# Performance work log

Measured on AMD Instinct MI355X. Metric: run time of the kernel, lower is better.

Reference implementation:

```python
import jax, jax.numpy as jnp
import numpy as np

N_HEADS = 16
PROJ_DIM = 64  # per-head dim
DIM = N_HEADS * PROJ_DIM  # 1024


def setup_inputs() -> dict:
    key = jax.random.key(0)
    k1, k2, k3, k4, k5 = jax.random.split(key, 5)
    N, L = 2, 2048
    scale = 1.0 / np.sqrt(DIM)
    return {
        "query": jax.random.normal(k1, (N, L, DIM), dtype=jnp.float32),
        "key": jax.random.normal(k2, (N, L, DIM), dtype=jnp.float32),
        "Wq": jax.random.normal(k3, (DIM, DIM), dtype=jnp.float32) * scale,
        "Wk": jax.random.normal(k4, (DIM, DIM), dtype=jnp.float32) * scale,
        "Wv": jax.random.normal(k5, (DIM, DIM), dtype=jnp.float32) * scale,
    }


def reference(query, key, Wq, Wk, Wv):
    # Causal linear-complexity attention (mask=True branch, left_first=False).
    N, Lq, _ = query.shape
    Lk = key.shape[1]
    H, Dh = N_HEADS, PROJ_DIM
    # torch Linear: x @ W.T ; reshape to (N, H, L, Dh)
    q = (query @ Wq.T).reshape(N, Lq, H, Dh).transpose(0, 2, 1, 3)
    k = (key @ Wk.T).reshape(N, Lk, H, Dh).transpose(0, 2, 1, 3)
    v = (key @ Wv.T).reshape(N, Lk, H, Dh).transpose(0, 2, 1, 3)
    q = jax.nn.softmax(q, axis=-1)
    k = jax.nn.softmax(k, axis=-1)
    # right[t] = sum_{s<=t} k_s^T v_s  : (N,H,Lk,Dh,Dh) cumulative outer products
    S = jnp.cumsum(jnp.einsum('nhti,nhtj->nhtij', k, v), axis=2)
    out = jnp.einsum('nhti,nhtij->nhtj', q, S)  # (N,H,Lq,Dh)
    return out.transpose(0, 2, 1, 3).reshape(N, Lq, H * Dh)
```

## Files before the change

kernel.cpp:

```cpp
#include <hip/hip_runtime.h>


constexpr int DIM  = 1024;
constexpr int H    = 16;
constexpr int DH   = 64;
constexpr int LSEQ = 2048;
constexpr int NB   = 2;
constexpr int MTOK = NB * LSEQ;
constexpr int CS   = 64;
constexpr int NC   = LSEQ / CS;

typedef __bf16 bf16x8 __attribute__((ext_vector_type(8)));
typedef float floatx4 __attribute__((ext_vector_type(4)));
typedef unsigned short ushort_t;

__device__ __forceinline__ ushort_t f2bf(float f) {
  unsigned int u = __float_as_uint(f);
  u += 0x7FFFu + ((u >> 16) & 1u);
  return (ushort_t)(u >> 16);
}

__device__ __forceinline__ void async16(void* lds, const void* g) {
  __builtin_amdgcn_global_load_lds(
      (const __attribute__((address_space(1))) unsigned int*)g,
      (__attribute__((address_space(3))) unsigned int*)lds, 16, 0, 0);
}

__device__ __forceinline__ bf16x8 tfrag(const unsigned int* T, int row, int uoff) {
  union { bf16x8 v; unsigned int u[4]; } r;
  const unsigned int* p = T + row * 33 + uoff;
  r.u[0] = p[0]; r.u[1] = p[1]; r.u[2] = p[2]; r.u[3] = p[3];
  return r.v;
}

__device__ __forceinline__ void transpose_tile(const ushort_t* g, unsigned int* TT, int tid) {
  const int ic = tid & 7, tp = tid >> 3;
  const ushort_t* r0 = g + (size_t)(2 * tp) * DIM + ic * 8;
  union { uint4 q; ushort_t u[8]; } a0, a1;
  a0.q = *(const uint4*)r0;
  a1.q = *(const uint4*)(r0 + DIM);
#pragma unroll
  for (int j = 0; j < 8; j++)
    TT[(8 * ic + j) * 33 + tp] = (unsigned int)a0.u[j] | ((unsigned int)a1.u[j] << 16);
}

__global__ __launch_bounds__(256) void cast_all(const float* __restrict__ q,
                                                const float* __restrict__ k,
                                                const float* __restrict__ wq,
                                                const float* __restrict__ wk,
                                                const float* __restrict__ wv,
                                                ushort_t* __restrict__ xbf,
                                                ushort_t* __restrict__ wbf) {
  const int seg = blockIdx.y;
  const float* src;
  ushort_t* dst;
  int n4;
  if (seg == 0)      { src = q;  dst = xbf;                  n4 = (4 << 20) / 4; }
  else if (seg == 1) { src = k;  dst = xbf + (4 << 20);      n4 = (4 << 20) / 4; }
  else if (seg == 2) { src = wq; dst = wbf;                  n4 = (1 << 20) / 4; }
  else if (seg == 3) { src = wk; dst = wbf + (1 << 20);      n4 = (1 << 20) / 4; }
  else               { src = wv; dst = wbf + (2 << 20);      n4 = (1 << 20) / 4; }
  for (int i = blockIdx.x * 256 + threadIdx.x; i < n4; i += gridDim.x * 256) {
    const float4 f = ((const float4*)src)[i];
    ((ushort4*)dst)[i] = make_ushort4(f2bf(f.x), f2bf(f.y), f2bf(f.z), f2bf(f.w));
  }
}

__global__ __launch_bounds__(512, 2) void gemm_fused(const ushort_t* __restrict__ xbf,
                                                     const ushort_t* __restrict__ wbf,
                                                     ushort_t* __restrict__ qp,
                                                     ushort_t* __restrict__ kp,
                                                     ushort_t* __restrict__ vp) {
  __shared__ __align__(16) ushort_t sh[65536];
  const int tid = threadIdx.x;

  const int xcd   = blockIdx.x & 7;
  const int local = blockIdx.x >> 3;
  const int T     = xcd * 24 + local;
  const int z     = T >> 6;
  const int rem   = T & 63;
  const int bm    = (rem >> 2) * 256;
  const int bn    = (rem & 3) * 256;

  const ushort_t* A = xbf + (z ? (size_t)(4 << 20) : 0);
  const ushort_t* W = wbf + (size_t)z * (1 << 20);
  ushort_t* C = (z == 0) ? qp : ((z == 1) ? kp : vp);

  const int lane  = tid & 63;
  const int wid   = tid >> 6;
  const int wr    = wid >> 2, wc = wid & 3;
  const int row16 = lane & 15, quad = lane >> 4;

  floatx4 acc[8][4] = {};

  const int srow = tid >> 3;
  const int lc   = (tid & 7) ^ (srow & 7);
  const ushort_t* pA[2][2];
  const ushort_t* pB[2][2];
#pragma unroll
  for (int h = 0; h < 2; h++)
#pragma unroll
    for (int rnd = 0; rnd < 2; rnd++) {
      pA[h][rnd] = A + (size_t)(bm + h * 128 + rnd * 64 + srow) * DIM + lc * 8;
      pB[h][rnd] = W + (size_t)(bn + h * 128 + rnd * 64 + srow) * DIM + lc * 8;
    }
  char* shW = (char*)sh;

#define STG(b, ism, h, kt)                                          \
  {                                                                 \
    char* d_ = shW + (b) * 65536 + (ism) * 32768 + (h) * 16384 + tid * 16; \
    async16(d_,        ((ism) ? pB : pA)[h][0] + (size_t)(kt) * 64);       \
    async16(d_ + 8192, ((ism) ? pB : pA)[h][1] + (size_t)(kt) * 64);       \
  }

  const int key = row16 & 7;
  const int xc0 = (quad ^ key) * 16;
  const int xc1 = ((4 + quad) ^ key) * 16;
  const int aOff = wr * 16384 + row16 * 128;
  const int bOff = 32768 + (wc >> 1) * 16384 + (wc & 1) * 8192 + row16 * 128;
  const char* shR = (const char*)sh;

  bf16x8 aF[4][2], bF[4][2];

#define RD_A4(p, base)                                                        \
  {                                                                           \
    _Pragma("unroll")                                                         \
    for (int mt = 0; mt < 4; mt++) {                                          \
      aF[mt][0] = *(const bf16x8*)(shR + (p) * 65536 + aOff + ((base) + mt) * 2048 + xc0); \
      aF[mt][1] = *(const bf16x8*)(shR + (p) * 65536 + aOff + ((base) + mt) * 2048 + xc1); \
    }                                                                         \
  }
#define RD_B2(p, base)                                                        \
  {                                                                           \
    _Pragma("unroll")                                                         \
    for (int j = 0; j < 2; j++) {                                             \
      bF[(base) + j][0] = *(const bf16x8*)(shR + (p) * 65536 + bOff + ((base) + j) * 2048 + xc0); \
      bF[(base) + j][1] = *(const bf16x8*)(shR + (p) * 65536 + bOff + ((base) + j) * 2048 + xc1); \
    }                                                                         \
  }
#define MFMA8(mb, nb)                                                         \
  {                                                                           \
    _Pragma("unroll")                                                         \
    for (int mt = 0; mt < 4; mt++)                                            \
      _Pragma("unroll")                                                       \
      for (int nt = 0; nt < 2; nt++) {                                        \
        acc[(mb) + mt][(nb) + nt] = __builtin_amdgcn_mfma_f32_16x16x32_bf16(  \
            aF[mt][0], bF[(nb) + nt][0], acc[(mb) + mt][(nb) + nt], 0, 0, 0); \
        acc[(mb) + mt][(nb) + nt] = __builtin_amdgcn_mfma_f32_16x16x32_bf16(  \
            aF[mt][1], bF[(nb) + nt][1], acc[(mb) + mt][(nb) + nt], 0, 0, 0); \
      }                                                                       \
  }
#define BARD()  asm volatile("s_barrier" ::: "memory")
#define LGKM0() asm volatile("s_waitcnt lgkmcnt(0)" ::: "memory")

  STG(0, 0, 0, 0); STG(0, 1, 0, 0);
  STG(0, 1, 1, 0); STG(0, 0, 1, 0);
  STG(1, 0, 0, 1); STG(1, 1, 0, 1);
  asm volatile("s_waitcnt vmcnt(4)" ::: "memory");
  BARD();

  for (int u = 0; u < 16; ++u) {
    const int p  = u & 1;
    const int qb = p ^ 1;
    RD_A4(p, 0); RD_B2(p, 0);
    if (u + 1 < 16) { STG(qb, 1, 1, u + 1); STG(qb, 0, 1, u + 1); }
    BARD(); LGKM0();
    __builtin_amdgcn_s_setprio(1); MFMA8(0, 0); __builtin_amdgcn_s_setprio(0);
    BARD();
    RD_B2(p, 2);
    BARD(); LGKM0();
    __builtin_amdgcn_s_setprio(1); MFMA8(0, 2); __builtin_amdgcn_s_setprio(0);
    BARD();
    RD_A4(p, 4);
    BARD(); LGKM0();
    __builtin_amdgcn_s_setprio(1); MFMA8(4, 0); __builtin_amdgcn_s_setprio(0);
    BARD();
    if (u + 2 < 16) {
      STG(p, 0, 0, u + 2); STG(p, 1, 0, u + 2);
      asm volatile("s_waitcnt vmcnt(4)" ::: "memory");
    } else {
      asm volatile("s_waitcnt vmcnt(0)" ::: "memory");
    }
    BARD();
    __builtin_amdgcn_s_setprio(1); MFMA8(4, 2); __builtin_amdgcn_s_setprio(0);
    BARD();
  }
#undef STG
#undef RD_A4
#undef RD_B2
#undef MFMA8
#undef BARD
#undef LGKM0
  __syncthreads();

  if (z < 2) {
#pragma unroll
    for (int mt = 0; mt < 8; mt++)
#pragma unroll
      for (int r = 0; r < 4; r++) {
        float m = fmaxf(fmaxf(acc[mt][0][r], acc[mt][1][r]),
                        fmaxf(acc[mt][2][r], acc[mt][3][r]));
#pragma unroll
        for (int o = 1; o < 16; o <<= 1) m = fmaxf(m, __shfl_xor(m, o, 64));
        float e[4], s = 0.f;
#pragma unroll
        for (int nt = 0; nt < 4; nt++) { e[nt] = __expf(acc[mt][nt][r] - m); s += e[nt]; }
#pragma unroll
        for (int o = 1; o < 16; o <<= 1) s += __shfl_xor(s, o, 64);
        const float inv = 1.f / s;
#pragma unroll
        for (int nt = 0; nt < 4; nt++) acc[mt][nt][r] = e[nt] * inv;
      }
  }

  ushort_t* CsB = sh;
#pragma unroll
  for (int p4 = 0; p4 < 4; ++p4) {
    __syncthreads();
    if (wr == (p4 >> 1)) {
      const int mh = (p4 & 1) * 4;
#pragma unroll
      for (int m4 = 0; m4 < 4; m4++)
#pragma unroll
        for (int nt = 0; nt < 4; nt++)
#pragma unroll
          for (int r = 0; r < 4; r++)
            CsB[(m4 * 16 + quad * 4 + r) * 264 + wc * 64 + nt * 16 + row16] =
                f2bf(acc[mh + m4][nt][r]);
    }
    __syncthreads();
#pragma unroll
    for (int it = 0; it < 4; it++) {
      const int ch = tid + it * 512;
      const int row = ch >> 5, ic = ch & 31;
      *(uint4*)&C[(size_t)(bm + p4 * 64 + row) * DIM + bn + ic * 8] =
          *(const uint4*)&CsB[row * 264 + ic * 8];
    }
  }
}

__global__ __launch_bounds__(256) void chunk_T(const ushort_t* __restrict__ kp,
                                               const ushort_t* __restrict__ vp,
                                               float* __restrict__ cs) {
  __shared__ unsigned int KT[64 * 33];
  __shared__ unsigned int VT[64 * 33];
  const int c = blockIdx.x, h = blockIdx.y, n = blockIdx.z;
  const int tid = threadIdx.x;
  const size_t gbase = ((size_t)(n * LSEQ + c * CS)) * DIM + h * DH;

  transpose_tile(kp + gbase, KT, tid);
  transpose_tile(vp + gbase, VT, tid);
  __syncthreads();

  const int lane = tid & 63, wid = tid >> 6;
  const int row16 = lane & 15, quad = lane >> 4;

  floatx4 acc[4] = {};
#pragma unroll
  for (int ks = 0; ks < 2; ks++) {
    const bf16x8 a = tfrag(VT, wid * 16 + row16, ks * 16 + quad * 4);
#pragma unroll
    for (int nt = 0; nt < 4; nt++) {
      const bf16x8 b = tfrag(KT, nt * 16 + row16, ks * 16 + quad * 4);
      acc[nt] = __builtin_amdgcn_mfma_f32_16x16x32_bf16(a, b, acc[nt], 0, 0, 0);
    }
  }
  float* outp = cs + ((size_t)((n * H + h) * NC + c)) * (DH * DH);
#pragma unroll
  for (int nt = 0; nt < 4; nt++)
#pragma unroll
    for (int r = 0; r < 4; r++)
      outp[(wid * 16 + quad * 4 + r) * DH + nt * 16 + row16] = acc[nt][r];
}

__global__ __launch_bounds__(256) void prefix_chunks(const float* __restrict__ cs,
                                                     ushort_t* __restrict__ csb) {
  const int nh = blockIdx.x >> 4;
  const int e  = (blockIdx.x & 15) * 256 + threadIdx.x;
  const float* bf_ = cs + (size_t)nh * NC * (DH * DH) + e;
  ushort_t* bb = csb + (size_t)nh * NC * (DH * DH) + e;
  float run = 0.f;
#pragma unroll
  for (int c = 0; c < NC; c++) {
    const float cur = bf_[(size_t)c * (DH * DH)];
    bb[(size_t)c * (DH * DH)] = f2bf(run);
    run += cur;
  }
}

__global__ __launch_bounds__(256) void attn_mfma(const ushort_t* __restrict__ qp,
                                                 const ushort_t* __restrict__ kp,
                                                 const ushort_t* __restrict__ vp,
                                                 const ushort_t* __restrict__ csb,
                                                 float* __restrict__ out) {
  __shared__ ushort_t Qs[64 * 72];
  __shared__ ushort_t Ks[64 * 72];
  __shared__ ushort_t Ts[64 * 72];
  __shared__ unsigned int VT[64 * 33];
  __shared__ ushort_t Pb[64 * 72];
  const int c = blockIdx.x, h = blockIdx.y, n = blockIdx.z;
  const int tid = threadIdx.x;
  const size_t gbase = ((size_t)(n * LSEQ + c * CS)) * DIM + h * DH;
  const size_t cbase = ((size_t)((n * H + h) * NC + c)) * (DH * DH);

#pragma unroll
  for (int it = 0; it < 2; it++) {
    const int ch = tid + it * 256;
    const int row = ch >> 3, ic = ch & 7;
    *(uint4*)&Qs[row * 72 + ic * 8] = *(const uint4*)&qp[gbase + (size_t)row * DIM + ic * 8];
    *(uint4*)&Ks[row * 72 + ic * 8] = *(const uint4*)&kp[gbase + (size_t)row * DIM + ic * 8];
    *(uint4*)&Ts[row * 72 + ic * 8] = *(const uint4*)&csb[cbase + (size_t)row * DH + ic * 8];
  }
  transpose_tile(vp + gbase, VT, tid);
  __syncthreads();

  const int lane = tid & 63, wid = tid >> 6;
  const int row16 = lane & 15, quad = lane >> 4;
  const int t0 = wid * 16;

  floatx4 acc[4] = {};
  floatx4 pacc[4] = {};

#pragma unroll
  for (int ks = 0; ks < 2; ks++) {
    const bf16x8 aq = *(const bf16x8*)&Qs[(t0 + row16) * 72 + ks * 32 + quad * 8];
#pragma unroll
    for (int nt = 0; nt < 4; nt++) {
      const bf16x8 bt = *(const bf16x8*)&Ts[(nt * 16 + row16) * 72 + ks * 32 + quad * 8];
      acc[nt] = __builtin_amdgcn_mfma_f32_16x16x32_bf16(aq, bt, acc[nt], 0, 0, 0);
      const bf16x8 bk = *(const bf16x8*)&Ks[(nt * 16 + row16) * 72 + ks * 32 + quad * 8];
      pacc[nt] = __builtin_amdgcn_mfma_f32_16x16x32_bf16(aq, bk, pacc[nt], 0, 0, 0);
    }
  }
#pragma unroll
  for (int nt = 0; nt < 4; nt++)
#pragma unroll
    for (int r = 0; r < 4; r++) {
      const int t = t0 + quad * 4 + r, s = nt * 16 + row16;
      Pb[t * 72 + s] = f2bf((s <= t) ? pacc[nt][r] : 0.f);
    }
  __syncthreads();

#pragma unroll
  for (int ks = 0; ks < 2; ks++) {
    const bf16x8 ap = *(const bf16x8*)&Pb[(t0 + row16) * 72 + ks * 32 + quad * 8];
#pragma unroll
    for (int nt = 0; nt < 4; nt++) {
      const bf16x8 bv = tfrag(VT, nt * 16 + row16, ks * 16 + quad * 4);
      acc[nt] = __builtin_amdgcn_mfma_f32_16x16x32_bf16(ap, bv, acc[nt], 0, 0, 0);
    }
  }

#pragma unroll
  for (int nt = 0; nt < 4; nt++)
#pragma unroll
    for (int r = 0; r < 4; r++)
      out[gbase + (size_t)(t0 + quad * 4 + r) * DIM + nt * 16 + row16] = acc[nt][r];
}

extern "C" void kernel_launch(void* const* d_in, const int* in_sizes, int n_in,
                              void* d_out, int out_size, void* d_ws, size_t ws_size,
                              hipStream_t stream) {
  const float* query = (const float*)d_in[0];
  const float* key   = (const float*)d_in[1];
  const float* Wq    = (const float*)d_in[2];
  const float* Wk    = (const float*)d_in[3];
  const float* Wv    = (const float*)d_in[4];
  float* out = (float*)d_out;

  const size_t PM = (size_t)4 << 20;
  ushort_t* qp = (ushort_t*)d_ws;
  ushort_t* kp = qp + PM;
  ushort_t* vp = kp + PM;
  float*    cs = (float*)(vp + PM);
  ushort_t* csb = (ushort_t*)(cs + PM);
  ushort_t* xbf = (ushort_t*)cs;
  ushort_t* wbf = (ushort_t*)out;

  cast_all<<<dim3(512, 5), 256, 0, stream>>>(query, key, Wq, Wk, Wv, xbf, wbf);

  gemm_fused<<<dim3(192), 512, 0, stream>>>(xbf, wbf, qp, kp, vp);

  chunk_T<<<dim3(NC, H, NB), 256, 0, stream>>>(kp, vp, cs);
  prefix_chunks<<<dim3(NB * H * 16), 256, 0, stream>>>(cs, csb);
  attn_mfma<<<dim3(NC, H, NB), 256, 0, stream>>>(qp, kp, vp, csb, out);
}
```

Baseline: 158.5 us.

## Simplify GEMM main loop to per-stage double buffering and batch prefix loads

```diff
diff --git a/kernel.cpp b/kernel.cpp
--- a/kernel.cpp
+++ b/kernel.cpp
@@ -106,12 +106,14 @@
     }
   char* shW = (char*)sh;
 
-#define STG(b, ism, h, kt)                                          \
+#define STG1(b, ism, h, kt)                                         \
   {                                                                 \
     char* d_ = shW + (b) * 65536 + (ism) * 32768 + (h) * 16384 + tid * 16; \
     async16(d_,        ((ism) ? pB : pA)[h][0] + (size_t)(kt) * 64);       \
     async16(d_ + 8192, ((ism) ? pB : pA)[h][1] + (size_t)(kt) * 64);       \
   }
+#define STG4(b, kt)                                                 \
+  { STG1(b, 0, 0, kt); STG1(b, 1, 0, kt); STG1(b, 0, 1, kt); STG1(b, 1, 1, kt); }
 
   const int key = row16 & 7;
   const int xc0 = (quad ^ key) * 16;
@@ -122,75 +124,66 @@
 
   bf16x8 aF[4][2], bF[4][2];
 
-#define RD_A4(p, base)                                                        \
+#define RD_A4(bp, base)                                                       \
   {                                                                           \
     _Pragma("unroll")                                                         \
     for (int mt = 0; mt < 4; mt++) {                                          \
-      aF[mt][0] = *(const bf16x8*)(shR + (p) * 65536 + aOff + ((base) + mt) * 2048 + xc0); \
-      aF[mt][1] = *(const bf16x8*)(shR + (p) * 65536 + aOff + ((base) + mt) * 2048 + xc1); \
+      aF[mt][0] = *(const bf16x8*)((bp) + aOff + ((base) + mt) * 2048 + xc0); \
+      aF[mt][1] = *(const bf16x8*)((bp) + aOff + ((base) + mt) * 2048 + xc1); \
     }                                                                         \
   }
-#define RD_B2(p, base)                                                        \
+#define RD_B4(bp)                                                             \
   {                                                                           \
     _Pragma("unroll")                                                         \
-    for (int j = 0; j < 2; j++) {                                             \
-      bF[(base) + j][0] = *(const bf16x8*)(shR + (p) * 65536 + bOff + ((base) + j) * 2048 + xc0); \
-      bF[(base) + j][1] = *(const bf16x8*)(shR + (p) * 65536 + bOff + ((base) + j) * 2048 + xc1); \
+    for (int j = 0; j < 4; j++) {                                             \
+      bF[j][0] = *(const bf16x8*)((bp) + bOff + j * 2048 + xc0);              \
+      bF[j][1] = *(const bf16x8*)((bp) + bOff + j * 2048 + xc1);              \
     }                                                                         \
   }
-#define MFMA8(mb, nb)                                                         \
+#define MFMA32(mb)                                                            \
   {                                                                           \
     _Pragma("unroll")                                                         \
     for (int mt = 0; mt < 4; mt++)                                            \
       _Pragma("unroll")                                                       \
-      for (int nt = 0; nt < 2; nt++) {                                        \
-        acc[(mb) + mt][(nb) + nt] = __builtin_amdgcn_mfma_f32_16x16x32_bf16(  \
-            aF[mt][0], bF[(nb) + nt][0], acc[(mb) + mt][(nb) + nt], 0, 0, 0); \
-        acc[(mb) + mt][(nb) + nt] = __builtin_amdgcn_mfma_f32_16x16x32_bf16(  \
-            aF[mt][1], bF[(nb) + nt][1], acc[(mb) + mt][(nb) + nt], 0, 0, 0); \
+      for (int nt = 0; nt < 4; nt++) {                                        \
+        acc[(mb) + mt][nt] = __builtin_amdgcn_mfma_f32_16x16x32_bf16(         \
+            aF[mt][0], bF[nt][0], acc[(mb) + mt][nt], 0, 0, 0);               \
+        acc[(mb) + mt][nt] = __builtin_amdgcn_mfma_f32_16x16x32_bf16(         \
+            aF[mt][1], bF[nt][1], acc[(mb) + mt][nt], 0, 0, 0);               \
       }                                                                       \
   }
-#define BARD()  asm volatile("s_barrier" ::: "memory")
-#define LGKM0() asm volatile("s_waitcnt lgkmcnt(0)" ::: "memory")
-
-  STG(0, 0, 0, 0); STG(0, 1, 0, 0);
-  STG(0, 1, 1, 0); STG(0, 0, 1, 0);
-  STG(1, 0, 0, 1); STG(1, 1, 0, 1);
-  asm volatile("s_waitcnt vmcnt(4)" ::: "memory");
-  BARD();
+
+  STG4(0, 0);
 
   for (int u = 0; u < 16; ++u) {
-    const int p  = u & 1;
-    const int qb = p ^ 1;
-    RD_A4(p, 0); RD_B2(p, 0);
-    if (u + 1 < 16) { STG(qb, 1, 1, u + 1); STG(qb, 0, 1, u + 1); }
-    BARD(); LGKM0();
-    __builtin_amdgcn_s_setprio(1); MFMA8(0, 0); __builtin_amdgcn_s_setprio(0);
-    BARD();
-    RD_B2(p, 2);
-    BARD(); LGKM0();
-    __builtin_amdgcn_s_setprio(1); MFMA8(0, 2); __builtin_amdgcn_s_setprio(0);
-    BARD();
-    RD_A4(p, 4);
-    BARD(); LGKM0();
-    __builtin_amdgcn_s_setprio(1); MFMA8(4, 0); __builtin_amdgcn_s_setprio(0);
-    BARD();
-    if (u + 2 < 16) {
-      STG(p, 0, 0, u + 2); STG(p, 1, 0, u + 2);
-      asm volatile("s_waitcnt vmcnt(4)" ::: "memory");
+    const int p = u & 1;
+    __builtin_amdgcn_sched_barrier(0);
+    asm volatile("s_waitcnt lgkmcnt(0)" ::: "memory");
+    __builtin_amdgcn_sched_barrier(0);
+    asm volatile("s_barrier" ::: "memory");
+    if (u + 1 < 16) {
+      STG4(p ^ 1, u + 1);
+      asm volatile("s_waitcnt vmcnt(8)" ::: "memory");
     } else {
       asm volatile("s_waitcnt vmcnt(0)" ::: "memory");
     }
-    BARD();
-    __builtin_amdgcn_s_setprio(1); MFMA8(4, 2); __builtin_amdgcn_s_setprio(0);
-    BARD();
-  }
-#undef STG
+    asm volatile("s_barrier" ::: "memory");
+    const char* bp = shR + p * 65536;
+    RD_A4(bp, 0);
+    RD_B4(bp);
+    __builtin_amdgcn_s_setprio(1);
+    MFMA32(0);
+    __builtin_amdgcn_s_setprio(0);
+    RD_A4(bp, 4);
+    __builtin_amdgcn_s_setprio(1);
+    MFMA32(4);
+    __builtin_amdgcn_s_setprio(0);
+  }
+#undef STG1
+#undef STG4
 #undef RD_A4
-#undef RD_B2
-#undef MFMA8
-#undef BARD
-#undef LGKM0
+#undef RD_B4
+#undef MFMA32
   __syncthreads();
 
   if (z < 2) {
@@ -279,12 +272,14 @@
   const int e  = (blockIdx.x & 15) * 256 + threadIdx.x;
   const float* bf_ = cs + (size_t)nh * NC * (DH * DH) + e;
   ushort_t* bb = csb + (size_t)nh * NC * (DH * DH) + e;
+  float v[NC];
+#pragma unroll
+  for (int c = 0; c < NC; c++) v[c] = bf_[(size_t)c * (DH * DH)];
   float run = 0.f;
 #pragma unroll
   for (int c = 0; c < NC; c++) {
-    const float cur = bf_[(size_t)c * (DH * DH)];
     bb[(size_t)c * (DH * DH)] = f2bf(run);
-    run += cur;
+    run += v[c];
   }
 }
 
```

New measurement: 159.0 us. No clear change (+0.3%).

## Replace chunk-prefix pass with two-level segmented scan fused into attention

Applied to the files above, without the earlier changes.

```diff
diff --git a/kernel.cpp b/kernel.cpp
--- a/kernel.cpp
+++ b/kernel.cpp
@@ -9,6 +9,8 @@
 constexpr int MTOK = NB * LSEQ;
 constexpr int CS   = 64;
 constexpr int NC   = LSEQ / CS;
+constexpr int SEG  = 8;
+constexpr int CPS  = NC / SEG;
 
 typedef __bf16 bf16x8 __attribute__((ext_vector_type(8)));
 typedef float floatx4 __attribute__((ext_vector_type(4)));
@@ -239,123 +241,159 @@
   }
 }
 
-__global__ __launch_bounds__(256) void chunk_T(const ushort_t* __restrict__ kp,
-                                               const ushort_t* __restrict__ vp,
-                                               float* __restrict__ cs) {
+__global__ __launch_bounds__(256) void seg_T(const ushort_t* __restrict__ kp,
+                                             const ushort_t* __restrict__ vp,
+                                             float* __restrict__ cs,
+                                             float* __restrict__ segtot) {
   __shared__ unsigned int KT[64 * 33];
   __shared__ unsigned int VT[64 * 33];
-  const int c = blockIdx.x, h = blockIdx.y, n = blockIdx.z;
+  const int s = blockIdx.x, h = blockIdx.y, n = blockIdx.z;
   const int tid = threadIdx.x;
-  const size_t gbase = ((size_t)(n * LSEQ + c * CS)) * DIM + h * DH;
-
-  transpose_tile(kp + gbase, KT, tid);
-  transpose_tile(vp + gbase, VT, tid);
-  __syncthreads();
-
   const int lane = tid & 63, wid = tid >> 6;
   const int row16 = lane & 15, quad = lane >> 4;
-
-  floatx4 acc[4] = {};
-#pragma unroll
-  for (int ks = 0; ks < 2; ks++) {
-    const bf16x8 a = tfrag(VT, wid * 16 + row16, ks * 16 + quad * 4);
-#pragma unroll
-    for (int nt = 0; nt < 4; nt++) {
-      const bf16x8 b = tfrag(KT, nt * 16 + row16, ks * 16 + quad * 4);
-      acc[nt] = __builtin_amdgcn_mfma_f32_16x16x32_bf16(a, b, acc[nt], 0, 0, 0);
-    }
-  }
-  float* outp = cs + ((size_t)((n * H + h) * NC + c)) * (DH * DH);
+  const int nh = n * H + h;
+
+  floatx4 run[4] = {};
+  for (int j = 0; j < CPS; j++) {
+    const int c = s * CPS + j;
+    const size_t gbase = ((size_t)(n * LSEQ + c * CS)) * DIM + h * DH;
+    if (j) __syncthreads();
+    transpose_tile(kp + gbase, KT, tid);
+    transpose_tile(vp + gbase, VT, tid);
+    __syncthreads();
+
+    floatx4 tacc[4] = {};
+#pragma unroll
+    for (int ks = 0; ks < 2; ks++) {
+      const bf16x8 a = tfrag(VT, wid * 16 + row16, ks * 16 + quad * 4);
+#pragma unroll
+      for (int nt = 0; nt < 4; nt++) {
+        const bf16x8 b = tfrag(KT, nt * 16 + row16, ks * 16 + quad * 4);
+        tacc[nt] = __builtin_amdgcn_mfma_f32_16x16x32_bf16(a, b, tacc[nt], 0, 0, 0);
+      }
+    }
+    float* outp = cs + ((size_t)(nh * NC + c)) * (DH * DH);
+#pragma unroll
+    for (int nt = 0; nt < 4; nt++)
+#pragma unroll
+      for (int r = 0; r < 4; r++)
+        outp[(wid * 16 + quad * 4 + r) * DH + nt * 16 + row16] = run[nt][r];
+#pragma unroll
+    for (int nt = 0; nt < 4; nt++) run[nt] += tacc[nt];
+  }
+  float* st = segtot + ((size_t)(nh * SEG + s)) * (DH * DH);
 #pragma unroll
   for (int nt = 0; nt < 4; nt++)
 #pragma unroll
     for (int r = 0; r < 4; r++)
-      outp[(wid * 16 + quad * 4 + r) * DH + nt * 16 + row16] = acc[nt][r];
-}
-
-__global__ __launch_bounds__(256) void prefix_chunks(const float* __restrict__ cs,
-                                                     ushort_t* __restrict__ csb) {
-  const int nh = blockIdx.x >> 4;
-  const int e  = (blockIdx.x & 15) * 256 + threadIdx.x;
-  const float* bf_ = cs + (size_t)nh * NC * (DH * DH) + e;
-  ushort_t* bb = csb + (size_t)nh * NC * (DH * DH) + e;
-  float run = 0.f;
-#pragma unroll
-  for (int c = 0; c < NC; c++) {
-    const float cur = bf_[(size_t)c * (DH * DH)];
-    bb[(size_t)c * (DH * DH)] = f2bf(run);
-    run += cur;
-  }
-}
-
-__global__ __launch_bounds__(256) void attn_mfma(const ushort_t* __restrict__ qp,
-                                                 const ushort_t* __restrict__ kp,
-                                                 const ushort_t* __restrict__ vp,
-                                                 const ushort_t* __restrict__ csb,
-                                                 float* __restrict__ out) {
-  __shared__ ushort_t Qs[64 * 72];
-  __shared__ ushort_t Ks[64 * 72];
-  __shared__ ushort_t Ts[64 * 72];
-  __shared__ unsigned int VT[64 * 33];
-  __shared__ ushort_t Pb[64 * 72];
-  const int c = blockIdx.x, h = blockIdx.y, n = blockIdx.z;
+      st[(wid * 16 + quad * 4 + r) * DH + nt * 16 + row16] = run[nt][r];
+}
+
+__global__ __launch_bounds__(512) void attn2(const ushort_t* __restrict__ qp,
+                                             const ushort_t* __restrict__ kp,
+                                             const ushort_t* __restrict__ vp,
+                                             const float* __restrict__ cs,
+                                             const float* __restrict__ segtot,
+                                             float* __restrict__ out) {
+  __shared__ float Sb[DH * DH];
+  __shared__ ushort_t Qs[2][64 * 72];
+  __shared__ ushort_t Ks[2][64 * 72];
+  __shared__ ushort_t Ts[2][64 * 72];
+  __shared__ ushort_t Pb[2][64 * 72];
+  __shared__ unsigned int VT2[2][64 * 33];
+  const int s = blockIdx.x, h = blockIdx.y, n = blockIdx.z;
   const int tid = threadIdx.x;
-  const size_t gbase = ((size_t)(n * LSEQ + c * CS)) * DIM + h * DH;
-  const size_t cbase = ((size_t)((n * H + h) * NC + c)) * (DH * DH);
-
-#pragma unroll
-  for (int it = 0; it < 2; it++) {
-    const int ch = tid + it * 256;
-    const int row = ch >> 3, ic = ch & 7;
-    *(uint4*)&Qs[row * 72 + ic * 8] = *(const uint4*)&qp[gbase + (size_t)row * DIM + ic * 8];
-    *(uint4*)&Ks[row * 72 + ic * 8] = *(const uint4*)&kp[gbase + (size_t)row * DIM + ic * 8];
-    *(uint4*)&Ts[row * 72 + ic * 8] = *(const uint4*)&csb[cbase + (size_t)row * DH + ic * 8];
-  }
-  transpose_tile(vp + gbase, VT, tid);
+  const int half = tid >> 8;
+  const int t8   = tid & 255;
+  const int lane = tid & 63;
+  const int wl   = (tid >> 6) & 3;
+  const int row16 = lane & 15, quad = lane >> 4;
+  const int nh = n * H + h;
+
+  {
+    float a8[8] = {0.f, 0.f, 0.f, 0.f, 0.f, 0.f, 0.f, 0.f};
+    const float* base = segtot + (size_t)nh * SEG * (DH * DH) + tid * 8;
+    for (int sp = 0; sp < s; sp++) {
+      const float4 u0 = *(const float4*)(base + (size_t)sp * (DH * DH));
+      const float4 u1 = *(const float4*)(base + (size_t)sp * (DH * DH) + 4);
+      a8[0] += u0.x; a8[1] += u0.y; a8[2] += u0.z; a8[3] += u0.w;
+      a8[4] += u1.x; a8[5] += u1.y; a8[6] += u1.z; a8[7] += u1.w;
+    }
+#pragma unroll
+    for (int i = 0; i < 8; i++) Sb[tid * 8 + i] = a8[i];
+  }
   __syncthreads();
 
-  const int lane = tid & 63, wid = tid >> 6;
-  const int row16 = lane & 15, quad = lane >> 4;
-  const int t0 = wid * 16;
-
-  floatx4 acc[4] = {};
-  floatx4 pacc[4] = {};
-
-#pragma unroll
-  for (int ks = 0; ks < 2; ks++) {
-    const bf16x8 aq = *(const bf16x8*)&Qs[(t0 + row16) * 72 + ks * 32 + quad * 8];
-#pragma unroll
-    for (int nt = 0; nt < 4; nt++) {
-      const bf16x8 bt = *(const bf16x8*)&Ts[(nt * 16 + row16) * 72 + ks * 32 + quad * 8];
-      acc[nt] = __builtin_amdgcn_mfma_f32_16x16x32_bf16(aq, bt, acc[nt], 0, 0, 0);
-      const bf16x8 bk = *(const bf16x8*)&Ks[(nt * 16 + row16) * 72 + ks * 32 + quad * 8];
-      pacc[nt] = __builtin_amdgcn_mfma_f32_16x16x32_bf16(aq, bk, pacc[nt], 0, 0, 0);
-    }
-  }
-#pragma unroll
-  for (int nt = 0; nt < 4; nt++)
-#pragma unroll
-    for (int r = 0; r < 4; r++) {
-      const int t = t0 + quad * 4 + r, s = nt * 16 + row16;
-      Pb[t * 72 + s] = f2bf((s <= t) ? pacc[nt][r] : 0.f);
-    }
-  __syncthreads();
-
-#pragma unroll
-  for (int ks = 0; ks < 2; ks++) {
-    const bf16x8 ap = *(const bf16x8*)&Pb[(t0 + row16) * 72 + ks * 32 + quad * 8];
-#pragma unroll
-    for (int nt = 0; nt < 4; nt++) {
-      const bf16x8 bv = tfrag(VT, nt * 16 + row16, ks * 16 + quad * 4);
-      acc[nt] = __builtin_amdgcn_mfma_f32_16x16x32_bf16(ap, bv, acc[nt], 0, 0, 0);
-    }
-  }
-
-#pragma unroll
-  for (int nt = 0; nt < 4; nt++)
-#pragma unroll
-    for (int r = 0; r < 4; r++)
-      out[gbase + (size_t)(t0 + quad * 4 + r) * DIM + nt * 16 + row16] = acc[nt][r];
+  for (int r2 = 0; r2 < 2; r2++) {
+    const int c = s * CPS + r2 * 2 + half;
+    const size_t gbase = ((size_t)(n * LSEQ + c * CS)) * DIM + h * DH;
+    const float* Pc = cs + ((size_t)(nh * NC + c)) * (DH * DH);
+    if (r2) __syncthreads();
+
+#pragma unroll
+    for (int it = 0; it < 2; it++) {
+      const int ch = t8 + it * 256;
+      const int row = ch >> 3, ic = ch & 7;
+      *(uint4*)&Qs[half][row * 72 + ic * 8] =
+          *(const uint4*)&qp[gbase + (size_t)row * DIM + ic * 8];
+      *(uint4*)&Ks[half][row * 72 + ic * 8] =
+          *(const uint4*)&kp[gbase + (size_t)row * DIM + ic * 8];
+    }
+    transpose_tile(vp + gbase, VT2[half], t8);
+#pragma unroll
+    for (int ii = 0; ii < 2; ii++) {
+      const int e = (t8 + ii * 256) * 8;
+      const int row = e >> 6, col = e & 63;
+      const float4 p0 = *(const float4*)(Pc + e);
+      const float4 p1 = *(const float4*)(Pc + e + 4);
+      ushort_t* d = &Ts[half][row * 72 + col];
+      *(ushort4*)d = make_ushort4(f2bf(p0.x + Sb[e]),     f2bf(p0.y + Sb[e + 1]),
+                                  f2bf(p0.z + Sb[e + 2]), f2bf(p0.w + Sb[e + 3]));
+      *(ushort4*)(d + 4) = make_ushort4(f2bf(p1.x + Sb[e + 4]), f2bf(p1.y + Sb[e + 5]),
+                                        f2bf(p1.z + Sb[e + 6]), f2bf(p1.w + Sb[e + 7]));
+    }
+    __syncthreads();
+
+    const int t0 = wl * 16;
+    floatx4 acc[4] = {};
+    floatx4 pacc[4] = {};
+
+#pragma unroll
+    for (int ks = 0; ks < 2; ks++) {
+      const bf16x8 aq = *(const bf16x8*)&Qs[half][(t0 + row16) * 72 + ks * 32 + quad * 8];
+#pragma unroll
+      for (int nt = 0; nt < 4; nt++) {
+        const bf16x8 bt = *(const bf16x8*)&Ts[half][(nt * 16 + row16) * 72 + ks * 32 + quad * 8];
+        acc[nt] = __builtin_amdgcn_mfma_f32_16x16x32_bf16(aq, bt, acc[nt], 0, 0, 0);
+        const bf16x8 bk = *(const bf16x8*)&Ks[half][(nt * 16 + row16) * 72 + ks * 32 + quad * 8];
+        pacc[nt] = __builtin_amdgcn_mfma_f32_16x16x32_bf16(aq, bk, pacc[nt], 0, 0, 0);
+      }
+    }
+#pragma unroll
+    for (int nt = 0; nt < 4; nt++)
+#pragma unroll
+      for (int r = 0; r < 4; r++) {
+        const int tt = t0 + quad * 4 + r, ss = nt * 16 + row16;
+        Pb[half][tt * 72 + ss] = f2bf((ss <= tt) ? pacc[nt][r] : 0.f);
+      }
+    __syncthreads();
+
+#pragma unroll
+    for (int ks = 0; ks < 2; ks++) {
+      const bf16x8 ap = *(const bf16x8*)&Pb[half][(t0 + row16) * 72 + ks * 32 + quad * 8];
+#pragma unroll
+      for (int nt = 0; nt < 4; nt++) {
+        const bf16x8 bv = tfrag(VT2[half], nt * 16 + row16, ks * 16 + quad * 4);
+        acc[nt] = __builtin_amdgcn_mfma_f32_16x16x32_bf16(ap, bv, acc[nt], 0, 0, 0);
+      }
+    }
+
+#pragma unroll
+    for (int nt = 0; nt < 4; nt++)
+#pragma unroll
+      for (int r = 0; r < 4; r++)
+        out[gbase + (size_t)(t0 + quad * 4 + r) * DIM + nt * 16 + row16] = acc[nt][r];
+  }
 }
 
 extern "C" void kernel_launch(void* const* d_in, const int* in_sizes, int n_in,
@@ -373,7 +411,7 @@
   ushort_t* kp = qp + PM;
   ushort_t* vp = kp + PM;
   float*    cs = (float*)(vp + PM);
-  ushort_t* csb = (ushort_t*)(cs + PM);
+  float*    segtot = cs + PM;
   ushort_t* xbf = (ushort_t*)cs;
   ushort_t* wbf = (ushort_t*)out;
 
@@ -381,7 +419,7 @@
 
   gemm_fused<<<dim3(192), 512, 0, stream>>>(xbf, wbf, qp, kp, vp);
 
-  chunk_T<<<dim3(NC, H, NB), 256, 0, stream>>>(kp, vp, cs);
-  prefix_chunks<<<dim3(NB * H * 16), 256, 0, stream>>>(cs, csb);
-  attn_mfma<<<dim3(NC, H, NB), 256, 0, stream>>>(qp, kp, vp, csb, out);
-}
+  seg_T<<<dim3(SEG, H, NB), 256, 0, stream>>>(kp, vp, cs, segtot);
+
+  attn2<<<dim3(SEG, H, NB), 512, 0, stream>>>(qp, kp, vp, cs, segtot, out);
+}
```

Measured after the change: 156.2 us (median of 2 runs). No clear change (-1.5%).

## Fuse chunk prefix sum into attention kernel by recomputing prior chunk states

Applied to the files above, without the earlier changes.

```diff
diff --git a/kernel.cpp b/kernel.cpp
--- a/kernel.cpp
+++ b/kernel.cpp
@@ -241,7 +241,7 @@
 
 __global__ __launch_bounds__(256) void chunk_T(const ushort_t* __restrict__ kp,
                                                const ushort_t* __restrict__ vp,
-                                               float* __restrict__ cs) {
+                                               float* __restrict__ ct) {
   __shared__ unsigned int KT[64 * 33];
   __shared__ unsigned int VT[64 * 33];
   const int c = blockIdx.x, h = blockIdx.y, n = blockIdx.z;
@@ -265,7 +265,7 @@
       acc[nt] = __builtin_amdgcn_mfma_f32_16x16x32_bf16(a, b, acc[nt], 0, 0, 0);
     }
   }
-  float* outp = cs + ((size_t)((n * H + h) * NC + c)) * (DH * DH);
+  float* outp = ct + ((size_t)((n * H + h) * NC + c)) * (DH * DH);
 #pragma unroll
   for (int nt = 0; nt < 4; nt++)
 #pragma unroll
@@ -273,35 +273,41 @@
       outp[(wid * 16 + quad * 4 + r) * DH + nt * 16 + row16] = acc[nt][r];
 }
 
-__global__ __launch_bounds__(256) void prefix_chunks(const float* __restrict__ cs,
-                                                     ushort_t* __restrict__ csb) {
-  const int nh = blockIdx.x >> 4;
-  const int e  = (blockIdx.x & 15) * 256 + threadIdx.x;
-  const float* bf_ = cs + (size_t)nh * NC * (DH * DH) + e;
-  ushort_t* bb = csb + (size_t)nh * NC * (DH * DH) + e;
-  float run = 0.f;
-#pragma unroll
-  for (int c = 0; c < NC; c++) {
-    const float cur = bf_[(size_t)c * (DH * DH)];
-    bb[(size_t)c * (DH * DH)] = f2bf(run);
-    run += cur;
-  }
-}
-
-__global__ __launch_bounds__(256) void attn_mfma(const ushort_t* __restrict__ qp,
-                                                 const ushort_t* __restrict__ kp,
-                                                 const ushort_t* __restrict__ vp,
-                                                 const ushort_t* __restrict__ csb,
-                                                 float* __restrict__ out) {
+__global__ __launch_bounds__(256) void attn4(const ushort_t* __restrict__ qp,
+                                             const ushort_t* __restrict__ kp,
+                                             const ushort_t* __restrict__ vp,
+                                             const float* __restrict__ ct,
+                                             float* __restrict__ out) {
   __shared__ ushort_t Qs[64 * 72];
   __shared__ ushort_t Ks[64 * 72];
   __shared__ ushort_t Ts[64 * 72];
+  __shared__ ushort_t Pb[64 * 72];
   __shared__ unsigned int VT[64 * 33];
-  __shared__ ushort_t Pb[64 * 72];
   const int c = blockIdx.x, h = blockIdx.y, n = blockIdx.z;
   const int tid = threadIdx.x;
+  const int lane = tid & 63, wid = tid >> 6;
+  const int row16 = lane & 15, quad = lane >> 4;
+  const int nh = n * H + h;
   const size_t gbase = ((size_t)(n * LSEQ + c * CS)) * DIM + h * DH;
-  const size_t cbase = ((size_t)((n * H + h) * NC + c)) * (DH * DH);
+
+  float sb[16] = {0.f, 0.f, 0.f, 0.f, 0.f, 0.f, 0.f, 0.f,
+                  0.f, 0.f, 0.f, 0.f, 0.f, 0.f, 0.f, 0.f};
+  {
+    const float* base = ct + (size_t)nh * NC * (DH * DH);
+    for (int cp = 0; cp < c; cp++) {
+      const float* bsp = base + (size_t)cp * (DH * DH);
+#pragma unroll
+      for (int ii = 0; ii < 2; ii++) {
+        const int e = (tid + ii * 256) * 8;
+        const float4 u0 = *(const float4*)(bsp + e);
+        const float4 u1 = *(const float4*)(bsp + e + 4);
+        sb[ii * 8 + 0] += u0.x; sb[ii * 8 + 1] += u0.y;
+        sb[ii * 8 + 2] += u0.z; sb[ii * 8 + 3] += u0.w;
+        sb[ii * 8 + 4] += u1.x; sb[ii * 8 + 5] += u1.y;
+        sb[ii * 8 + 6] += u1.z; sb[ii * 8 + 7] += u1.w;
+      }
+    }
+  }
 
 #pragma unroll
   for (int it = 0; it < 2; it++) {
@@ -309,15 +315,21 @@
     const int row = ch >> 3, ic = ch & 7;
     *(uint4*)&Qs[row * 72 + ic * 8] = *(const uint4*)&qp[gbase + (size_t)row * DIM + ic * 8];
     *(uint4*)&Ks[row * 72 + ic * 8] = *(const uint4*)&kp[gbase + (size_t)row * DIM + ic * 8];
-    *(uint4*)&Ts[row * 72 + ic * 8] = *(const uint4*)&csb[cbase + (size_t)row * DH + ic * 8];
   }
   transpose_tile(vp + gbase, VT, tid);
+#pragma unroll
+  for (int ii = 0; ii < 2; ii++) {
+    const int e = (tid + ii * 256) * 8;
+    const int row = e >> 6, col = e & 63;
+    ushort_t* d = &Ts[row * 72 + col];
+    *(ushort4*)d = make_ushort4(f2bf(sb[ii * 8 + 0]), f2bf(sb[ii * 8 + 1]),
+                                f2bf(sb[ii * 8 + 2]), f2bf(sb[ii * 8 + 3]));
+    *(ushort4*)(d + 4) = make_ushort4(f2bf(sb[ii * 8 + 4]), f2bf(sb[ii * 8 + 5]),
+                                      f2bf(sb[ii * 8 + 6]), f2bf(sb[ii * 8 + 7]));
+  }
   __syncthreads();
 
-  const int lane = tid & 63, wid = tid >> 6;
-  const int row16 = lane & 15, quad = lane >> 4;
   const int t0 = wid * 16;
-
   floatx4 acc[4] = {};
   floatx4 pacc[4] = {};
 
@@ -336,8 +348,8 @@
   for (int nt = 0; nt < 4; nt++)
 #pragma unroll
     for (int r = 0; r < 4; r++) {
-      const int t = t0 + quad * 4 + r, s = nt * 16 + row16;
-      Pb[t * 72 + s] = f2bf((s <= t) ? pacc[nt][r] : 0.f);
+      const int tt = t0 + quad * 4 + r, ss = nt * 16 + row16;
+      Pb[tt * 72 + ss] = f2bf((ss <= tt) ? pacc[nt][r] : 0.f);
     }
   __syncthreads();
 
@@ -372,16 +384,15 @@
   ushort_t* qp = (ushort_t*)d_ws;
   ushort_t* kp = qp + PM;
   ushort_t* vp = kp + PM;
-  float*    cs = (float*)(vp + PM);
-  ushort_t* csb = (ushort_t*)(cs + PM);
-  ushort_t* xbf = (ushort_t*)cs;
+  float*    ct = (float*)(vp + PM);
+  ushort_t* xbf = (ushort_t*)ct;
   ushort_t* wbf = (ushort_t*)out;
 
   cast_all<<<dim3(512, 5), 256, 0, stream>>>(query, key, Wq, Wk, Wv, xbf, wbf);
 
   gemm_fused<<<dim3(192), 512, 0, stream>>>(xbf, wbf, qp, kp, vp);
 
-  chunk_T<<<dim3(NC, H, NB), 256, 0, stream>>>(kp, vp, cs);
-  prefix_chunks<<<dim3(NB * H * 16), 256, 0, stream>>>(cs, csb);
-  attn_mfma<<<dim3(NC, H, NB), 256, 0, stream>>>(qp, kp, vp, csb, out);
-}
+  chunk_T<<<dim3(NC, H, NB), 256, 0, stream>>>(kp, vp, ct);
+
+  attn4<<<dim3(NC, H, NB), 256, 0, stream>>>(qp, kp, vp, ct, out);
+}
```

Result: slower. 177.9 us (+12.3%).
